# Kernel optimization log

Measured on AMD Instinct MI355X. Metric: run time of the kernel, lower is better.

## Reference

```python
import jax, jax.numpy as jnp
import numpy as np

MARGIN = 2.0


def setup_inputs() -> dict:
    key = jax.random.key(0)
    k1, k2 = jax.random.split(key)
    B, D, NUM_CLASSES = 8192, 128, 100
    features = jax.random.normal(k1, (B, D), dtype=jnp.float32)
    labels = jax.random.randint(k2, (B,), 0, NUM_CLASSES, dtype=jnp.int64)
    return {"features": features, "labels": labels}


def reference(features, labels):
    # Vectorized form of the O(B^2) nested-loop contrastive loss.
    B = features.shape[0]
    sq = jnp.sum(features * features, axis=-1)                      # [B]
    # squared pairwise L2 distances via the gram matrix
    d2 = sq[:, None] + sq[None, :] - 2.0 * (features @ features.T)  # [B, B]
    d2 = jnp.maximum(d2, 0.0)

    off_diag = ~jnp.eye(B, dtype=bool)
    same = labels[:, None] == labels[None, :]
    pos_mask = same & off_diag
    neg_mask = (~same) & off_diag

    # positive pairs contribute squared distance
    pos_loss = jnp.sum(jnp.where(pos_mask, d2, 0.0))

    # negative pairs contribute clamp(margin - dist, 0)^2; guard sqrt(0) grads
    d = jnp.sqrt(jnp.where(neg_mask, d2, 1.0))
    hinge = jnp.maximum(MARGIN - d, 0.0)
    neg_loss = jnp.sum(jnp.where(neg_mask, hinge * hinge, 0.0))

    pos_count = jnp.sum(pos_mask)
    total_pairs = jnp.asarray(B * (B - 1), dtype=d2.dtype)
    loss = pos_loss + neg_loss
    # original divides only when positive_pairs > 0
    return jnp.where(pos_count > 0, loss / total_pairs, loss)
```

## Files before the change

### kernel.cpp

```cpp
#include <hip/hip_runtime.h>
#include <hip/hip_bf16.h>


#define BN 8192
#define DD 128
#define NTILES 64
#define NBLOCKS (NTILES * (NTILES + 1) / 2)
#define SQ 26.0f
#define INV_S2 (1.0f / (26.0f * 26.0f))
#define D2I_HINGE 2704
#define D2I_BIG 0x7fffffff

typedef __attribute__((ext_vector_type(4))) int i32x4;

__global__ __launch_bounds__(256) void prep_kernel(const float* __restrict__ f,
        const int* __restrict__ labels, char* __restrict__ fbp,
        int2* __restrict__ meta) {
    const int tid = threadIdx.x;
    const int p = blockIdx.x;
    __shared__ __align__(16) char ls[16][144];

    const int r = tid >> 4;
    const int c = (tid & 15) * 8;
    const float* src = f + ((size_t)p * 16 + r) * DD + c;
    float4 a = *(const float4*)src;
    float4 b = *(const float4*)(src + 4);
    float rv[8] = {a.x, a.y, a.z, a.w, b.x, b.y, b.z, b.w};
    int s = 0;
#pragma unroll
    for (int j = 0; j < 8; j++) {
        int q = __float2int_rn(fminf(fmaxf(rv[j] * SQ, -127.f), 127.f));
        ls[r][c + j] = (char)q;
        s += q * q;
    }
#pragma unroll
    for (int off = 8; off > 0; off >>= 1) s += __shfl_down(s, off, 16);
    if ((tid & 15) == 0) meta[p * 16 + r] = make_int2(s, labels[p * 16 + r]);
    __syncthreads();

    if (tid < 128) {
        const int ks = tid >> 6, lane = tid & 63;
        const int l15 = lane & 15, quad = lane >> 4;
        i32x4 pack = *(const i32x4*)&ls[l15][ks * 64 + quad * 16];
        *(i32x4*)(fbp + ((size_t)(p * 2 + ks) * 64 + lane) * 16) = pack;
    }
}

__global__ __launch_bounds__(256) void pair_kernel(
        const char* __restrict__ fbp, const int2* __restrict__ meta,
        float2* __restrict__ partial) {
    const int t = blockIdx.x;
    int by = (int)((sqrtf(8.f * (float)t + 1.f) - 1.f) * 0.5f);
    while ((by + 1) * (by + 2) / 2 <= t) by++;
    while (by * (by + 1) / 2 > t) by--;
    const int bx = t - by * (by + 1) / 2;
    const bool diag = (bx == by);

    const int tid = threadIdx.x;
    const int wave = tid >> 6, lane = tid & 63;
    const int wx = wave & 1, wy = wave >> 1;
    const int i0 = bx * 128 + wy * 64;
    const int j0 = by * 128 + wx * 64;
    const int ip = i0 >> 4, jp = j0 >> 4;
    const int l15 = lane & 15, quad = lane >> 4;

    float pos = 0.f, neg = 0.f;

    if (!(diag && wx < wy)) {
        i32x4 acc4[4][4];
#pragma unroll
        for (int a = 0; a < 4; a++)
#pragma unroll
            for (int b = 0; b < 4; b++) acc4[a][b] = (i32x4){0, 0, 0, 0};

#pragma unroll
        for (int ks = 0; ks < 2; ks++) {
            i32x4 af[4], bg[4];
#pragma unroll
            for (int tt = 0; tt < 4; tt++)
                af[tt] = *(const i32x4*)(fbp +
                    ((size_t)((ip + tt) * 2 + ks) * 64 + lane) * 16);
#pragma unroll
            for (int tt = 0; tt < 4; tt++)
                bg[tt] = *(const i32x4*)(fbp +
                    ((size_t)((jp + tt) * 2 + ks) * 64 + lane) * 16);
#pragma unroll
            for (int m = 0; m < 4; m++)
#pragma unroll
                for (int n = 0; n < 4; n++)
                    acc4[m][n] = __builtin_amdgcn_mfma_i32_16x16x64_i8(
                        af[m], bg[n], acc4[m][n], 0, 0, 0);
        }

        int2 mj[4];
#pragma unroll
        for (int ni = 0; ni < 4; ni++) mj[ni] = meta[j0 + ni * 16 + l15];
        int2 mi[4][4];
#pragma unroll
        for (int m = 0; m < 4; m++)
#pragma unroll
            for (int r = 0; r < 4; r++) mi[m][r] = meta[i0 + m * 16 + quad * 4 + r];

        const bool strict = diag && (wx == wy);
        int posi = 0, dmin = D2I_BIG;
#pragma unroll
        for (int m = 0; m < 4; m++)
#pragma unroll
            for (int n = 0; n < 4; n++)
#pragma unroll
                for (int r = 0; r < 4; r++) {
                    int il = m * 16 + quad * 4 + r;
                    int jl = n * 16 + l15;
                    bool valid = !strict || (il < jl);
                    bool same = mi[m][r].y == mj[n].y;
                    int d2i = mi[m][r].x + mj[n].x - 2 * acc4[m][n][r];
                    posi += (valid && same) ? d2i : 0;
                    dmin = min(dmin, (valid && !same) ? d2i : D2I_BIG);
                }
        pos = (float)posi * INV_S2;

        if (__any(dmin < D2I_HINGE)) {
#pragma unroll
            for (int m = 0; m < 4; m++)
#pragma unroll
                for (int n = 0; n < 4; n++)
#pragma unroll
                    for (int r = 0; r < 4; r++) {
                        int il = m * 16 + quad * 4 + r;
                        int jl = n * 16 + l15;
                        bool valid = !strict || (il < jl);
                        bool sameL = mi[m][r].y == mj[n].y;
                        int d2i = mi[m][r].x + mj[n].x - 2 * acc4[m][n][r];
                        float d2 = (float)d2i * INV_S2;
                        if (valid && !sameL && d2 < 4.0f) {
                            float h = 2.0f - sqrtf(d2);
                            neg += h * h;
                        }
                    }
        }
    }

#pragma unroll
    for (int off = 32; off > 0; off >>= 1) {
        pos += __shfl_down(pos, off, 64);
        neg += __shfl_down(neg, off, 64);
    }
    __shared__ float red[2][4];
    if (lane == 0) { red[0][wave] = pos; red[1][wave] = neg; }
    __syncthreads();
    if (tid == 0)
        partial[t] = make_float2(red[0][0] + red[0][1] + red[0][2] + red[0][3],
                                 red[1][0] + red[1][1] + red[1][2] + red[1][3]);
}

__global__ __launch_bounds__(256) void reduce_kernel(
        const float2* __restrict__ partial, float* __restrict__ out) {
    const int tid = threadIdx.x;
    float p = 0.f, n = 0.f;
    for (int i = tid; i < NBLOCKS; i += 256) {
        float2 v = partial[i];
        p += v.x; n += v.y;
    }
#pragma unroll
    for (int off = 32; off > 0; off >>= 1) {
        p += __shfl_down(p, off, 64);
        n += __shfl_down(n, off, 64);
    }
    __shared__ float red[2][4];
    int lane = tid & 63, w = tid >> 6;
    if (lane == 0) { red[0][w] = p; red[1][w] = n; }
    __syncthreads();
    if (tid == 0) {
        float total = 2.0f * (red[0][0] + red[0][1] + red[0][2] + red[0][3] +
                              red[1][0] + red[1][1] + red[1][2] + red[1][3]);
        out[0] = total / 67100672.0f;
    }
}

extern "C" void kernel_launch(void* const* d_in, const int* in_sizes, int n_in,
                              void* d_out, int out_size, void* d_ws, size_t ws_size,
                              hipStream_t stream) {
    const float* f = (const float*)d_in[0];
    const int* labels = (const int*)d_in[1];
    float* out = (float*)d_out;

    char* fbp = (char*)d_ws;
    int2* meta = (int2*)((char*)d_ws + (size_t)BN * DD);
    float2* partial = (float2*)(meta + BN);

    prep_kernel<<<BN / 16, 256, 0, stream>>>(f, labels, fbp, meta);
    pair_kernel<<<NBLOCKS, 256, 0, stream>>>(fbp, meta, partial);
    reduce_kernel<<<1, 256, 0, stream>>>(partial, out);
}
```

Measured before the change: 79.48 us.

## Compute positive-pair loss algebraically from per-class sums instead of per-pair

```diff
diff --git a/kernel.cpp b/kernel.cpp
--- a/kernel.cpp
+++ b/kernel.cpp
@@ -7,18 +7,23 @@
 #define NTILES 64
 #define NBLOCKS (NTILES * (NTILES + 1) / 2)
 #define SQ 26.0f
-#define INV_S2 (1.0f / (26.0f * 26.0f))
+#define INV_S2 (1.0 / (26.0 * 26.0))
+#define INV_S2F (1.0f / (26.0f * 26.0f))
 #define D2I_HINGE 2704
 #define D2I_BIG 0x7fffffff
+#define NCLS 100
 
 typedef __attribute__((ext_vector_type(4))) int i32x4;
 
 __global__ __launch_bounds__(256) void prep_kernel(const float* __restrict__ f,
         const int* __restrict__ labels, char* __restrict__ fbp,
-        int2* __restrict__ meta) {
+        int* __restrict__ normv, int* __restrict__ csum_g) {
     const int tid = threadIdx.x;
     const int p = blockIdx.x;
     __shared__ __align__(16) char ls[16][144];
+
+    if (p == 0)
+        for (int k = tid; k < NCLS * DD; k += 256) csum_g[k] = 0;
 
     const int r = tid >> 4;
     const int c = (tid & 15) * 8;
@@ -35,7 +40,7 @@
     }
 #pragma unroll
     for (int off = 8; off > 0; off >>= 1) s += __shfl_down(s, off, 16);
-    if ((tid & 15) == 0) meta[p * 16 + r] = make_int2(s, labels[p * 16 + r]);
+    if ((tid & 15) == 0) normv[p * 16 + r] = s;
     __syncthreads();
 
     if (tid < 128) {
@@ -46,9 +51,39 @@
     }
 }
 
+__global__ __launch_bounds__(256) void csum_kernel(const float* __restrict__ f,
+        const int* __restrict__ labels, int* __restrict__ csum_g) {
+    __shared__ int lcs[NCLS * DD];
+    const int tid = threadIdx.x;
+    for (int k = tid; k < NCLS * DD; k += 256) lcs[k] = 0;
+    __syncthreads();
+
+    const int r0 = blockIdx.x * 256;
+    const int rr = tid >> 4;
+    const int c = (tid & 15) * 8;
+    for (int it = 0; it < 16; it++) {
+        const int row = r0 + it * 16 + rr;
+        const float* src = f + (size_t)row * DD + c;
+        float4 a = *(const float4*)src;
+        float4 b = *(const float4*)(src + 4);
+        float rv[8] = {a.x, a.y, a.z, a.w, b.x, b.y, b.z, b.w};
+        int* dst = &lcs[labels[row] * DD + c];
+#pragma unroll
+        for (int j = 0; j < 8; j++) {
+            int q = __float2int_rn(fminf(fmaxf(rv[j] * SQ, -127.f), 127.f));
+            atomicAdd(&dst[j], q);
+        }
+    }
+    __syncthreads();
+    for (int k = tid; k < NCLS * DD; k += 256) {
+        int v = lcs[k];
+        if (v) atomicAdd(&csum_g[k], v);
+    }
+}
+
 __global__ __launch_bounds__(256) void pair_kernel(
-        const char* __restrict__ fbp, const int2* __restrict__ meta,
-        float2* __restrict__ partial) {
+        const char* __restrict__ fbp, const int* __restrict__ normv,
+        const int* __restrict__ labels, float* __restrict__ partial) {
     const int t = blockIdx.x;
     int by = (int)((sqrtf(8.f * (float)t + 1.f) - 1.f) * 0.5f);
     while ((by + 1) * (by + 2) / 2 <= t) by++;
@@ -64,7 +99,7 @@
     const int ip = i0 >> 4, jp = j0 >> 4;
     const int l15 = lane & 15, quad = lane >> 4;
 
-    float pos = 0.f, neg = 0.f;
+    float neg = 0.f;
 
     if (!(diag && wx < wy)) {
         i32x4 acc4[4][4];
@@ -92,34 +127,53 @@
                         af[m], bg[n], acc4[m][n], 0, 0, 0);
         }
 
-        int2 mj[4];
-#pragma unroll
-        for (int ni = 0; ni < 4; ni++) mj[ni] = meta[j0 + ni * 16 + l15];
-        int2 mi[4][4];
+        int wn[4];
+#pragma unroll
+        for (int n = 0; n < 4; n++) wn[n] = normv[j0 + n * 16 + l15];
+        int un[4][4];
 #pragma unroll
         for (int m = 0; m < 4; m++)
 #pragma unroll
-            for (int r = 0; r < 4; r++) mi[m][r] = meta[i0 + m * 16 + quad * 4 + r];
+            for (int r = 0; r < 4; r++)
+                un[m][r] = normv[i0 + m * 16 + quad * 4 + r];
 
         const bool strict = diag && (wx == wy);
-        int posi = 0, dmin = D2I_BIG;
-#pragma unroll
-        for (int m = 0; m < 4; m++)
-#pragma unroll
-            for (int n = 0; n < 4; n++)
+        int dmin = D2I_BIG;
+        if (!strict) {
+#pragma unroll
+            for (int m = 0; m < 4; m++)
+#pragma unroll
+                for (int r = 0; r < 4; r++) {
+                    int s_mr = un[m][r];
+#pragma unroll
+                    for (int n = 0; n < 4; n++)
+                        dmin = min(dmin, s_mr + wn[n] - 2 * acc4[m][n][r]);
+                }
+        } else {
+#pragma unroll
+            for (int m = 0; m < 4; m++)
 #pragma unroll
                 for (int r = 0; r < 4; r++) {
                     int il = m * 16 + quad * 4 + r;
-                    int jl = n * 16 + l15;
-                    bool valid = !strict || (il < jl);
-                    bool same = mi[m][r].y == mj[n].y;
-                    int d2i = mi[m][r].x + mj[n].x - 2 * acc4[m][n][r];
-                    posi += (valid && same) ? d2i : 0;
-                    dmin = min(dmin, (valid && !same) ? d2i : D2I_BIG);
+#pragma unroll
+                    for (int n = 0; n < 4; n++) {
+                        int jl = n * 16 + l15;
+                        int d2i = un[m][r] + wn[n] - 2 * acc4[m][n][r];
+                        dmin = min(dmin, (il < jl) ? d2i : D2I_BIG);
+                    }
                 }
-        pos = (float)posi * INV_S2;
+        }
 
         if (__any(dmin < D2I_HINGE)) {
+            int lj[4];
+#pragma unroll
+            for (int n = 0; n < 4; n++) lj[n] = labels[j0 + n * 16 + l15];
+            int li[4][4];
+#pragma unroll
+            for (int m = 0; m < 4; m++)
+#pragma unroll
+                for (int r = 0; r < 4; r++)
+                    li[m][r] = labels[i0 + m * 16 + quad * 4 + r];
 #pragma unroll
             for (int m = 0; m < 4; m++)
 #pragma unroll
@@ -129,11 +183,9 @@
                         int il = m * 16 + quad * 4 + r;
                         int jl = n * 16 + l15;
                         bool valid = !strict || (il < jl);
-                        bool sameL = mi[m][r].y == mj[n].y;
-                        int d2i = mi[m][r].x + mj[n].x - 2 * acc4[m][n][r];
-                        float d2 = (float)d2i * INV_S2;
-                        if (valid && !sameL && d2 < 4.0f) {
-                            float h = 2.0f - sqrtf(d2);
+                        int d2i = un[m][r] + wn[n] - 2 * acc4[m][n][r];
+                        if (valid && li[m][r] != lj[n] && d2i < D2I_HINGE) {
+                            float h = 2.0f - sqrtf((float)d2i * INV_S2F);
                             neg += h * h;
                         }
                     }
@@ -141,39 +193,52 @@
     }
 
 #pragma unroll
-    for (int off = 32; off > 0; off >>= 1) {
-        pos += __shfl_down(pos, off, 64);
-        neg += __shfl_down(neg, off, 64);
-    }
-    __shared__ float red[2][4];
-    if (lane == 0) { red[0][wave] = pos; red[1][wave] = neg; }
-    __syncthreads();
-    if (tid == 0)
-        partial[t] = make_float2(red[0][0] + red[0][1] + red[0][2] + red[0][3],
-                                 red[1][0] + red[1][1] + red[1][2] + red[1][3]);
+    for (int off = 32; off > 0; off >>= 1) neg += __shfl_down(neg, off, 64);
+    __shared__ float red[4];
+    if (lane == 0) red[wave] = neg;
+    __syncthreads();
+    if (tid == 0) partial[t] = red[0] + red[1] + red[2] + red[3];
 }
 
 __global__ __launch_bounds__(256) void reduce_kernel(
-        const float2* __restrict__ partial, float* __restrict__ out) {
-    const int tid = threadIdx.x;
-    float p = 0.f, n = 0.f;
-    for (int i = tid; i < NBLOCKS; i += 256) {
-        float2 v = partial[i];
-        p += v.x; n += v.y;
-    }
-#pragma unroll
-    for (int off = 32; off > 0; off >>= 1) {
-        p += __shfl_down(p, off, 64);
-        n += __shfl_down(n, off, 64);
-    }
-    __shared__ float red[2][4];
-    int lane = tid & 63, w = tid >> 6;
-    if (lane == 0) { red[0][w] = p; red[1][w] = n; }
+        const float* __restrict__ partial, const int* __restrict__ normv,
+        const int* __restrict__ labels, const int* __restrict__ csum_g,
+        float* __restrict__ out) {
+    const int tid = threadIdx.x;
+    __shared__ int cnt[NCLS];
+    __shared__ int snorm[NCLS];
+    __shared__ double posc[NCLS];
+    __shared__ float redn[4];
+
+    if (tid < NCLS) { cnt[tid] = 0; snorm[tid] = 0; }
+    __syncthreads();
+    for (int i = tid; i < BN; i += 256) {
+        int l = labels[i];
+        atomicAdd(&cnt[l], 1);
+        atomicAdd(&snorm[l], normv[i]);
+    }
+    __syncthreads();
+    if (tid < NCLS) {
+        long long cc = 0;
+        const int* cs = &csum_g[tid * DD];
+        for (int d = 0; d < DD; d++) { long long v = cs[d]; cc += v * v; }
+        posc[tid] = (double)(2LL * ((long long)cnt[tid] * (long long)snorm[tid] - cc));
+    }
+    __syncthreads();
+
+    float nsum = 0.f;
+    for (int i = tid; i < NBLOCKS; i += 256) nsum += partial[i];
+#pragma unroll
+    for (int off = 32; off > 0; off >>= 1) nsum += __shfl_down(nsum, off, 64);
+    const int lane = tid & 63, w = tid >> 6;
+    if (lane == 0) redn[w] = nsum;
     __syncthreads();
     if (tid == 0) {
-        float total = 2.0f * (red[0][0] + red[0][1] + red[0][2] + red[0][3] +
-                              red[1][0] + red[1][1] + red[1][2] + red[1][3]);
-        out[0] = total / 67100672.0f;
+        double pos = 0.0;
+        for (int c = 0; c < NCLS; c++) pos += posc[c];
+        double neg = (double)(redn[0] + redn[1] + redn[2] + redn[3]);
+        double total = pos * INV_S2 + 2.0 * neg;
+        out[0] = (float)(total / 67100672.0);
     }
 }
 
@@ -185,10 +250,12 @@
     float* out = (float*)d_out;
 
     char* fbp = (char*)d_ws;
-    int2* meta = (int2*)((char*)d_ws + (size_t)BN * DD);
-    float2* partial = (float2*)(meta + BN);
-
-    prep_kernel<<<BN / 16, 256, 0, stream>>>(f, labels, fbp, meta);
-    pair_kernel<<<NBLOCKS, 256, 0, stream>>>(fbp, meta, partial);
-    reduce_kernel<<<1, 256, 0, stream>>>(partial, out);
-}
+    int* normv = (int*)((char*)d_ws + (size_t)BN * DD);
+    float* partial = (float*)(normv + BN);
+    int* csum_g = (int*)(partial + NBLOCKS);
+
+    prep_kernel<<<BN / 16, 256, 0, stream>>>(f, labels, fbp, normv, csum_g);
+    csum_kernel<<<32, 256, 0, stream>>>(f, labels, csum_g);
+    pair_kernel<<<NBLOCKS, 256, 0, stream>>>(fbp, normv, labels, partial);
+    reduce_kernel<<<1, 256, 0, stream>>>(partial, normv, labels, csum_g, out);
+}
```

Result: slower. 99.81 us (+25.6%).

## Pair two upper-triangle tiles per block and specialize non-diagonal masking

Applied to the files above, without the earlier changes.

```diff
diff --git a/kernel.cpp b/kernel.cpp
--- a/kernel.cpp
+++ b/kernel.cpp
@@ -5,11 +5,12 @@
 #define BN 8192
 #define DD 128
 #define NTILES 64
-#define NBLOCKS (NTILES * (NTILES + 1) / 2)
+#define NPBLK 1056
 #define SQ 26.0f
-#define INV_S2 (1.0f / (26.0f * 26.0f))
+#define INV_S2F (1.0f / (26.0f * 26.0f))
 #define D2I_HINGE 2704
 #define D2I_BIG 0x7fffffff
+#define PROW(v) ((((v) + 1) * ((v) + 1)) >> 2)
 
 typedef __attribute__((ext_vector_type(4))) int i32x4;
 
@@ -49,29 +50,40 @@
 __global__ __launch_bounds__(256) void pair_kernel(
         const char* __restrict__ fbp, const int2* __restrict__ meta,
         float2* __restrict__ partial) {
-    const int t = blockIdx.x;
-    int by = (int)((sqrtf(8.f * (float)t + 1.f) - 1.f) * 0.5f);
-    while ((by + 1) * (by + 2) / 2 <= t) by++;
-    while (by * (by + 1) / 2 > t) by--;
-    const int bx = t - by * (by + 1) / 2;
-    const bool diag = (bx == by);
+    const int b = blockIdx.x;
+    int by = (int)(2.0f * sqrtf((float)b + 1.0f)) - 1;
+    by = max(0, min(63, by));
+    while (PROW(by) > b) by--;
+    while (PROW(by + 1) <= b) by++;
+    const int a = b - PROW(by);
 
     const int tid = threadIdx.x;
     const int wave = tid >> 6, lane = tid & 63;
     const int wx = wave & 1, wy = wave >> 1;
-    const int i0 = bx * 128 + wy * 64;
     const int j0 = by * 128 + wx * 64;
-    const int ip = i0 >> 4, jp = j0 >> 4;
+    const int jp = j0 >> 4;
     const int l15 = lane & 15, quad = lane >> 4;
 
+    int2 mj[4];
+#pragma unroll
+    for (int ni = 0; ni < 4; ni++) mj[ni] = meta[j0 + ni * 16 + l15];
+
     float pos = 0.f, neg = 0.f;
 
-    if (!(diag && wx < wy)) {
+    for (int half = 0; half < 2; ++half) {
+        const int bx = 2 * a + half;
+        if (bx > by) break;
+        const bool diag = (bx == by);
+        if (diag && wx < wy) continue;
+
+        const int i0 = bx * 128 + wy * 64;
+        const int ip = i0 >> 4;
+
         i32x4 acc4[4][4];
 #pragma unroll
-        for (int a = 0; a < 4; a++)
-#pragma unroll
-            for (int b = 0; b < 4; b++) acc4[a][b] = (i32x4){0, 0, 0, 0};
+        for (int aa = 0; aa < 4; aa++)
+#pragma unroll
+            for (int bb = 0; bb < 4; bb++) acc4[aa][bb] = (i32x4){0, 0, 0, 0};
 
 #pragma unroll
         for (int ks = 0; ks < 2; ks++) {
@@ -92,32 +104,43 @@
                         af[m], bg[n], acc4[m][n], 0, 0, 0);
         }
 
-        int2 mj[4];
-#pragma unroll
-        for (int ni = 0; ni < 4; ni++) mj[ni] = meta[j0 + ni * 16 + l15];
         int2 mi[4][4];
 #pragma unroll
         for (int m = 0; m < 4; m++)
 #pragma unroll
-            for (int r = 0; r < 4; r++) mi[m][r] = meta[i0 + m * 16 + quad * 4 + r];
+            for (int r = 0; r < 4; r++)
+                mi[m][r] = meta[i0 + m * 16 + quad * 4 + r];
 
         const bool strict = diag && (wx == wy);
         int posi = 0, dmin = D2I_BIG;
-#pragma unroll
-        for (int m = 0; m < 4; m++)
-#pragma unroll
-            for (int n = 0; n < 4; n++)
-#pragma unroll
-                for (int r = 0; r < 4; r++) {
-                    int il = m * 16 + quad * 4 + r;
-                    int jl = n * 16 + l15;
-                    bool valid = !strict || (il < jl);
-                    bool same = mi[m][r].y == mj[n].y;
-                    int d2i = mi[m][r].x + mj[n].x - 2 * acc4[m][n][r];
-                    posi += (valid && same) ? d2i : 0;
-                    dmin = min(dmin, (valid && !same) ? d2i : D2I_BIG);
-                }
-        pos = (float)posi * INV_S2;
+        if (!strict) {
+#pragma unroll
+            for (int m = 0; m < 4; m++)
+#pragma unroll
+                for (int n = 0; n < 4; n++)
+#pragma unroll
+                    for (int r = 0; r < 4; r++) {
+                        int d2i = mi[m][r].x + mj[n].x - 2 * acc4[m][n][r];
+                        posi += (mi[m][r].y == mj[n].y) ? d2i : 0;
+                        dmin = min(dmin, d2i);
+                    }
+        } else {
+#pragma unroll
+            for (int m = 0; m < 4; m++)
+#pragma unroll
+                for (int n = 0; n < 4; n++)
+#pragma unroll
+                    for (int r = 0; r < 4; r++) {
+                        int il = m * 16 + quad * 4 + r;
+                        int jl = n * 16 + l15;
+                        bool valid = il < jl;
+                        bool same = mi[m][r].y == mj[n].y;
+                        int d2i = mi[m][r].x + mj[n].x - 2 * acc4[m][n][r];
+                        posi += (valid && same) ? d2i : 0;
+                        dmin = min(dmin, valid ? d2i : D2I_BIG);
+                    }
+        }
+        pos += (float)posi * INV_S2F;
 
         if (__any(dmin < D2I_HINGE)) {
 #pragma unroll
@@ -131,9 +154,8 @@
                         bool valid = !strict || (il < jl);
                         bool sameL = mi[m][r].y == mj[n].y;
                         int d2i = mi[m][r].x + mj[n].x - 2 * acc4[m][n][r];
-                        float d2 = (float)d2i * INV_S2;
-                        if (valid && !sameL && d2 < 4.0f) {
-                            float h = 2.0f - sqrtf(d2);
+                        if (valid && !sameL && d2i < D2I_HINGE) {
+                            float h = 2.0f - sqrtf((float)d2i * INV_S2F);
                             neg += h * h;
                         }
                     }
@@ -149,7 +171,7 @@
     if (lane == 0) { red[0][wave] = pos; red[1][wave] = neg; }
     __syncthreads();
     if (tid == 0)
-        partial[t] = make_float2(red[0][0] + red[0][1] + red[0][2] + red[0][3],
+        partial[b] = make_float2(red[0][0] + red[0][1] + red[0][2] + red[0][3],
                                  red[1][0] + red[1][1] + red[1][2] + red[1][3]);
 }
 
@@ -157,7 +179,7 @@
         const float2* __restrict__ partial, float* __restrict__ out) {
     const int tid = threadIdx.x;
     float p = 0.f, n = 0.f;
-    for (int i = tid; i < NBLOCKS; i += 256) {
+    for (int i = tid; i < NPBLK; i += 256) {
         float2 v = partial[i];
         p += v.x; n += v.y;
     }
@@ -189,6 +211,6 @@
     float2* partial = (float2*)(meta + BN);
 
     prep_kernel<<<BN / 16, 256, 0, stream>>>(f, labels, fbp, meta);
-    pair_kernel<<<NBLOCKS, 256, 0, stream>>>(fbp, meta, partial);
+    pair_kernel<<<NPBLK, 256, 0, stream>>>(fbp, meta, partial);
     reduce_kernel<<<1, 256, 0, stream>>>(partial, out);
 }
```

Measured after the change: 82.16 us. 1.03x slower.
